# Optimization experiments

Measured on AMD Instinct MI355X. Metric: run time of the kernel, lower is better.

## Reference

```python
import jax, jax.numpy as jnp
import numpy as np

D = 1024
H = 16
HD = D // H
FF = 4 * D
EPS = 1e-5


def _layernorm(x, scale, shift):
    # Faithful to the torch module: unbiased std (ddof=1), eps added to std.
    mean = jnp.mean(x, axis=-1, keepdims=True)
    var = jnp.sum((x - mean) ** 2, axis=-1, keepdims=True) / (x.shape[-1] - 1)
    std = jnp.sqrt(var)
    return shift + scale * (x - mean) / (std + EPS)


def _gelu(x):
    c = jnp.sqrt(jnp.asarray(2.0 / jnp.pi, dtype=x.dtype))
    return 0.5 * x * (1.0 + jnp.tanh(c * (x + 0.044715 * x ** 3)))


def setup_inputs() -> dict:
    key = jax.random.key(0)
    ks = jax.random.split(key, 8)
    B, S = 2, 2048
    inv = 1.0 / np.sqrt(D)
    x = jax.random.normal(ks[0], (B, S, D), dtype=jnp.float32)
    scale1 = jnp.ones((D,), jnp.float32)
    shift1 = jnp.zeros((D,), jnp.float32)
    Wqkv = jax.random.normal(ks[1], (3 * D, D), jnp.float32) * inv  # torch layout [out,in]
    Wo_w = jax.random.normal(ks[2], (D, D), jnp.float32) * inv
    Wo_b = jnp.zeros((D,), jnp.float32)
    scale2 = jnp.ones((D,), jnp.float32)
    shift2 = jnp.zeros((D,), jnp.float32)
    W1 = jax.random.normal(ks[3], (FF, D), jnp.float32) * inv
    b1 = jnp.zeros((FF,), jnp.float32)
    W2 = jax.random.normal(ks[4], (D, FF), jnp.float32) * (1.0 / np.sqrt(FF))
    b2 = jnp.zeros((D,), jnp.float32)
    return {"x": x, "scale1": scale1, "shift1": shift1, "Wqkv": Wqkv,
            "Wo_w": Wo_w, "Wo_b": Wo_b, "scale2": scale2, "shift2": shift2,
            "W1": W1, "b1": b1, "W2": W2, "b2": b2}


def reference(x, scale1, shift1, Wqkv, Wo_w, Wo_b, scale2, shift2, W1, b1, W2, b2):
    B, S, _ = x.shape
    # --- pre-norm attention ---
    h = _layernorm(x, scale1, shift1)
    qkv = jnp.einsum('bsd,ed->bse', h, Wqkv)  # [B,S,3D]
    q, k, v = jnp.split(qkv, 3, axis=-1)
    q = q.reshape(B, S, H, HD).transpose(0, 2, 1, 3)  # [B,H,S,HD]
    k = k.reshape(B, S, H, HD).transpose(0, 2, 1, 3)
    v = v.reshape(B, S, H, HD).transpose(0, 2, 1, 3)
    scores = jnp.einsum('bhqd,bhkd->bhqk', q, k) / jnp.sqrt(jnp.asarray(HD, x.dtype))
    causal = jnp.triu(jnp.ones((S, S), dtype=bool), k=1)
    scores = jnp.where(causal, -jnp.inf, scores)
    weights = jax.nn.softmax(scores, axis=-1)
    attn = jnp.einsum('bhqk,bhkd->bhqd', weights, v)
    attn = attn.transpose(0, 2, 1, 3).reshape(B, S, D)
    attn = jnp.einsum('bsd,ed->bse', attn, Wo_w) + Wo_b
    x = x + attn
    # --- pre-norm MLP ---
    h2 = _layernorm(x, scale2, shift2)
    m = _gelu(jnp.einsum('bsd,fd->bsf', h2, W1) + b1)
    m = jnp.einsum('bsf,df->bsd', m, W2) + b2
    return x + m
```

## Files before the change

kernel.cpp:

```cpp
#include <hip/hip_runtime.h>
#include <cstdint>
#include <cstddef>

typedef __bf16 bf16;
typedef __bf16 v8bf __attribute__((ext_vector_type(8)));
typedef __bf16 v4bf __attribute__((ext_vector_type(4)));
typedef float  v4f  __attribute__((ext_vector_type(4)));

#define D_MODEL 1024
#define FF_DIM  4096
#define SEQ     2048
#define NTOK    4096
#define NH      16
#define HDIM    64

#define GLOAD_LDS16(g, l) \
    __builtin_amdgcn_global_load_lds((const __attribute__((address_space(1))) void*)(g), \
                                     (__attribute__((address_space(3))) void*)(l), 16, 0, 0)

#define QSCALE 0.18033688011112042f
#define SHIFT2 -28.853900817779268f

#define BARRIER()    asm volatile("s_barrier" ::: "memory")
#define WAIT_VM8()   asm volatile("s_waitcnt vmcnt(8)" ::: "memory")
#define WAIT_VM0()   asm volatile("s_waitcnt vmcnt(0)" ::: "memory")
#define WAIT_LGKM0() asm volatile("s_waitcnt lgkmcnt(0)" ::: "memory")

__global__ __launch_bounds__(256) void prep_kernel(
    const float* __restrict__ Wqkv, const float* __restrict__ Wo,
    const float* __restrict__ W1, const float* __restrict__ W2,
    bf16* __restrict__ Wqkv_b, bf16* __restrict__ Wo_b,
    bf16* __restrict__ W1_b, bf16* __restrict__ W2_b) {
    int u = blockIdx.x * 256 + threadIdx.x;
    const float* src; bf16* dst; int idx;
    if (u < 786432)       { src = Wqkv; dst = Wqkv_b; idx = u * 4; }
    else if (u < 1048576) { src = Wo;   dst = Wo_b;   idx = (u - 786432) * 4; }
    else if (u < 2097152) { src = W1;   dst = W1_b;   idx = (u - 1048576) * 4; }
    else                  { src = W2;   dst = W2_b;   idx = (u - 2097152) * 4; }
    float4 v = *(const float4*)(src + idx);
    dst[idx + 0] = (bf16)v.x;
    dst[idx + 1] = (bf16)v.y;
    dst[idx + 2] = (bf16)v.z;
    dst[idx + 3] = (bf16)v.w;
}

__global__ __launch_bounds__(256) void layernorm_kernel(
    const float* __restrict__ x, const float* __restrict__ scale,
    const float* __restrict__ shift, bf16* __restrict__ out) {
    int row = blockIdx.x;
    int t = threadIdx.x;
    const float* xr = x + (size_t)row * D_MODEL;
    float4 v = *(const float4*)(xr + t * 4);
    float s  = v.x + v.y + v.z + v.w;
    float sq = v.x * v.x + v.y * v.y + v.z * v.z + v.w * v.w;
    #pragma unroll
    for (int o = 1; o < 64; o <<= 1) {
        s  += __shfl_xor(s, o);
        sq += __shfl_xor(sq, o);
    }
    __shared__ float ws[8];
    int wv = t >> 6;
    if ((t & 63) == 0) { ws[wv * 2] = s; ws[wv * 2 + 1] = sq; }
    __syncthreads();
    s  = ws[0] + ws[2] + ws[4] + ws[6];
    sq = ws[1] + ws[3] + ws[5] + ws[7];
    float mean = s * (1.0f / D_MODEL);
    float var  = (sq - (float)D_MODEL * mean * mean) * (1.0f / (D_MODEL - 1));
    var = fmaxf(var, 0.0f);
    float inv = 1.0f / (sqrtf(var) + 1e-5f);
    #pragma unroll
    for (int j = 0; j < 4; ++j) {
        int c = t * 4 + j;
        float xv = (&v.x)[j];
        out[(size_t)row * D_MODEL + c] = (bf16)(shift[c] + scale[c] * (xv - mean) * inv);
    }
}

__global__ __launch_bounds__(256) void transpose_v(
    const bf16* __restrict__ vb, bf16* __restrict__ vt) {
    int bh = blockIdx.x >> 5;
    int ts = blockIdx.x & 31;
    int t = threadIdx.x;
    __shared__ bf16 T[64][72];
    const bf16* src = vb + ((size_t)bh * SEQ + ts * 64) * HDIM;
    #pragma unroll
    for (int half = 0; half < 2; ++half) {
        int s = (t >> 3) + half * 32;
        int d0 = (t & 7) * 8;
        v8bf vv = *(const v8bf*)(src + (size_t)s * HDIM + d0);
        #pragma unroll
        for (int j = 0; j < 8; ++j) T[d0 + j][s] = vv[j];
    }
    __syncthreads();
    bf16* dst = vt + (size_t)bh * HDIM * SEQ + ts * 64;
    int d = t >> 2;
    #pragma unroll
    for (int cc = 0; cc < 2; ++cc) {
        int c = (t & 3) + cc * 4;
        v8bf o = *(const v8bf*)(&T[d][c * 8]);
        *(v8bf*)(dst + (size_t)d * SEQ + c * 8) = o;
    }
}

template <int EPI>
__global__ __launch_bounds__(256) void gemm_nt(
    const bf16* __restrict__ A, const bf16* __restrict__ Bw,
    const float* __restrict__ bias, const float* __restrict__ resid,
    float* __restrict__ outf, bf16* __restrict__ ob0,
    bf16* __restrict__ ob1, bf16* __restrict__ ob2,
    int M, int N, int K, int klen) {
    __shared__ __align__(16) bf16 As[128 * 64];
    __shared__ __align__(16) bf16 Bs[128 * 64];
    int gx = gridDim.x;
    int lin = blockIdx.y * gx + blockIdx.x;
    int grpsz = 16 * gx;
    int group = lin / grpsz;
    int rem = lin - group * grpsz;
    int m_t = group * 16 + (rem & 15);
    int n_t = rem >> 4;
    int m0 = m_t * 128, n0 = n_t * 128;
    int kstart = blockIdx.z * klen;
    int t = threadIdx.x;
    int lane = t & 63, wave = t >> 6;
    int wm = wave >> 1, wn = wave & 1;
    int quad = lane >> 4, l16 = lane & 15;

    int srow8 = lane >> 3;
    int schunk = (lane & 7) ^ srow8;
    const bf16* agp = A  + (size_t)(m0 + wave * 8 + srow8) * K + kstart + schunk * 8;
    const bf16* bgp = Bw + (size_t)(n0 + wave * 8 + srow8) * K + kstart + schunk * 8;
    size_t row32 = (size_t)32 * K;

    v4f acc[4][4];
    #pragma unroll
    for (int i = 0; i < 4; ++i)
        #pragma unroll
        for (int j = 0; j < 4; ++j)
            acc[i][j] = (v4f){0.f, 0.f, 0.f, 0.f};

    int rsw = l16 & 7;
    for (int kk = 0; kk < klen; kk += 64) {
        __syncthreads();
        #pragma unroll
        for (int ii = 0; ii < 4; ++ii) {
            GLOAD_LDS16(agp + ii * row32 + kk, &As[ii * 2048 + wave * 512]);
            GLOAD_LDS16(bgp + ii * row32 + kk, &Bs[ii * 2048 + wave * 512]);
        }
        __syncthreads();
        #pragma unroll
        for (int h = 0; h < 2; ++h) {
            v8bf af[4], bfr[4];
            #pragma unroll
            for (int i = 0; i < 4; ++i)
                af[i] = *(const v8bf*)(&As[(wm * 64 + i * 16 + l16) * 64 + (((h * 4 + quad) ^ rsw)) * 8]);
            #pragma unroll
            for (int j = 0; j < 4; ++j)
                bfr[j] = *(const v8bf*)(&Bs[(wn * 64 + j * 16 + l16) * 64 + (((h * 4 + quad) ^ rsw)) * 8]);
            #pragma unroll
            for (int i = 0; i < 4; ++i)
                #pragma unroll
                for (int j = 0; j < 4; ++j)
                    acc[i][j] = __builtin_amdgcn_mfma_f32_16x16x32_bf16(af[i], bfr[j], acc[i][j], 0, 0, 0);
        }
    }

    #pragma unroll
    for (int i = 0; i < 4; ++i) {
        #pragma unroll
        for (int j = 0; j < 4; ++j) {
            #pragma unroll
            for (int r = 0; r < 4; ++r) {
                float v = acc[i][j][r];
                int row = m0 + wm * 64 + i * 16 + quad * 4 + r;
                int col = n0 + wn * 64 + j * 16 + l16;
                if (EPI == 1) {
                    size_t o = (size_t)row * N + col;
                    outf[o] = resid[o] + v + bias[col];
                }
            }
        }
    }
}

template <int EPI>
__global__ __launch_bounds__(512, 2) void gemm2_nt(
    const bf16* __restrict__ A, const bf16* __restrict__ Bw,
    const float* __restrict__ bias, bf16* __restrict__ ob0,
    bf16* __restrict__ ob1, bf16* __restrict__ ob2,
    int M, int N, int K, int klen) {
    __shared__ __align__(16) bf16 smA[2][256 * 64];
    __shared__ __align__(16) bf16 smB[2][256 * 64];

    int m0 = blockIdx.y * 256, n0 = blockIdx.x * 256;
    int kstart = blockIdx.z * klen;
    int t = threadIdx.x;
    int lane = t & 63, wave = t >> 6;
    int wm = wave >> 2, wn = wave & 3;
    int quad = lane >> 4, l16 = lane & 15;

    int srow8 = lane >> 3;
    int schunk = (lane & 7) ^ srow8;
    const bf16* aA = A  + (size_t)(m0 + wave * 8 + srow8) * K + kstart + schunk * 8;
    const bf16* bB = Bw + (size_t)(n0 + wave * 8 + srow8) * K + kstart + schunk * 8;
    size_t row64 = (size_t)64 * K;
    int NT = klen >> 6;

    v4f acc[8][4];
    #pragma unroll
    for (int i = 0; i < 8; ++i)
        #pragma unroll
        for (int j = 0; j < 4; ++j)
            acc[i][j] = (v4f){0.f, 0.f, 0.f, 0.f};

    auto stage = [&](int c, int kt) {
        size_t ko = (size_t)kt * 64;
        const bf16* ag = aA + ko;
        const bf16* bg = bB + ko;
        #pragma unroll
        for (int q = 0; q < 4; ++q) {
            GLOAD_LDS16(ag + q * row64, &smA[c][q * 4096 + wave * 512]);
            GLOAD_LDS16(bg + q * row64, &smB[c][q * 4096 + wave * 512]);
        }
    };

    stage(0, 0);
    if (NT > 1) { stage(1, 1); WAIT_VM8(); } else { WAIT_VM0(); }
    BARRIER();

    int rx = l16 & 7;
    int ch0 = (quad ^ rx) * 8;
    int ch1 = ch0 ^ 32;
    int arow = (wm * 128 + l16) * 64;
    int brow = (wn * 64 + l16) * 64;

    for (int kt = 0; kt < NT; ++kt) {
        int c = kt & 1;
        const bf16* Ab = &smA[c][arow];
        const bf16* Bb = &smB[c][brow];
        v8bf a[4][2], b[4][2];
        #pragma unroll
        for (int i = 0; i < 4; ++i) {
            a[i][0] = *(const v8bf*)(Ab + i * 1024 + ch0);
            a[i][1] = *(const v8bf*)(Ab + i * 1024 + ch1);
        }
        #pragma unroll
        for (int j = 0; j < 4; ++j) {
            b[j][0] = *(const v8bf*)(Bb + j * 1024 + ch0);
            b[j][1] = *(const v8bf*)(Bb + j * 1024 + ch1);
        }
        __builtin_amdgcn_s_setprio(1);
        #pragma unroll
        for (int i = 0; i < 4; ++i)
            #pragma unroll
            for (int j = 0; j < 2; ++j) {
                acc[i][j] = __builtin_amdgcn_mfma_f32_16x16x32_bf16(a[i][0], b[j][0], acc[i][j], 0, 0, 0);
                acc[i][j] = __builtin_amdgcn_mfma_f32_16x16x32_bf16(a[i][1], b[j][1], acc[i][j], 0, 0, 0);
            }
        __builtin_amdgcn_s_setprio(0);
        __builtin_amdgcn_s_setprio(1);
        #pragma unroll
        for (int i = 0; i < 4; ++i)
            #pragma unroll
            for (int j = 2; j < 4; ++j) {
                acc[i][j] = __builtin_amdgcn_mfma_f32_16x16x32_bf16(a[i][0], b[j][0], acc[i][j], 0, 0, 0);
                acc[i][j] = __builtin_amdgcn_mfma_f32_16x16x32_bf16(a[i][1], b[j][1], acc[i][j], 0, 0, 0);
            }
        __builtin_amdgcn_s_setprio(0);
        #pragma unroll
        for (int i = 0; i < 4; ++i) {
            a[i][0] = *(const v8bf*)(Ab + 4096 + i * 1024 + ch0);
            a[i][1] = *(const v8bf*)(Ab + 4096 + i * 1024 + ch1);
        }
        __builtin_amdgcn_s_setprio(1);
        #pragma unroll
        for (int i = 0; i < 4; ++i)
            #pragma unroll
            for (int j = 0; j < 2; ++j) {
                acc[i + 4][j] = __builtin_amdgcn_mfma_f32_16x16x32_bf16(a[i][0], b[j][0], acc[i + 4][j], 0, 0, 0);
                acc[i + 4][j] = __builtin_amdgcn_mfma_f32_16x16x32_bf16(a[i][1], b[j][1], acc[i + 4][j], 0, 0, 0);
            }
        __builtin_amdgcn_s_setprio(0);
        WAIT_LGKM0();
        BARRIER();
        if (kt + 2 < NT) stage(c, kt + 2);
        __builtin_amdgcn_s_setprio(1);
        #pragma unroll
        for (int i = 0; i < 4; ++i)
            #pragma unroll
            for (int j = 2; j < 4; ++j) {
                acc[i + 4][j] = __builtin_amdgcn_mfma_f32_16x16x32_bf16(a[i][0], b[j][0], acc[i + 4][j], 0, 0, 0);
                acc[i + 4][j] = __builtin_amdgcn_mfma_f32_16x16x32_bf16(a[i][1], b[j][1], acc[i + 4][j], 0, 0, 0);
            }
        __builtin_amdgcn_s_setprio(0);
        if (kt + 1 < NT) {
            if (kt + 2 < NT) WAIT_VM8();
            else             WAIT_VM0();
            BARRIER();
        }
    }

    #pragma unroll
    for (int i = 0; i < 8; ++i) {
        #pragma unroll
        for (int j = 0; j < 4; ++j) {
            #pragma unroll
            for (int r = 0; r < 4; ++r) {
                float v = acc[i][j][r];
                int row = m0 + wm * 128 + i * 16 + quad * 4 + r;
                int col = n0 + wn * 64 + j * 16 + l16;
                if (EPI == 0) {
                    int which = col >> 10, rr = col & 1023;
                    int h = rr >> 6, d = rr & 63;
                    int bb = row >> 11, sI = row & 2047;
                    size_t dst = (((size_t)(bb * NH + h)) * SEQ + sI) * HDIM + d;
                    if (which == 0)      ob0[dst] = (bf16)(v * QSCALE);
                    else if (which == 1) ob1[dst] = (bf16)v;
                    else                 ob2[dst] = (bf16)v;
                } else if (EPI == 2) {
                    float u = v + bias[col];
                    float y = 1.5957691216057308f * (u + 0.044715f * u * u * u);
                    float g = u * __builtin_amdgcn_rcpf(1.0f + __expf(-y));
                    ob0[(size_t)row * N + col] = (bf16)g;
                } else {
                    ob0[(size_t)blockIdx.z * M * N + (size_t)row * N + col] = (bf16)v;
                }
            }
        }
    }
}

__global__ __launch_bounds__(256) void combine_w2(
    const bf16* __restrict__ part, const float* __restrict__ x1,
    const float* __restrict__ b2, float* __restrict__ out) {
    int i = (blockIdx.x * 256 + threadIdx.x) * 4;
    int col = i & (D_MODEL - 1);
    float4 xv = *(const float4*)(x1 + i);
    float4 bv = *(const float4*)(b2 + col);
    float4 r;
    r.x = xv.x + bv.x; r.y = xv.y + bv.y; r.z = xv.z + bv.z; r.w = xv.w + bv.w;
    #pragma unroll
    for (int z = 0; z < 4; ++z) {
        v4bf p = *(const v4bf*)(part + (size_t)z * NTOK * D_MODEL + i);
        r.x += (float)p[0]; r.y += (float)p[1]; r.z += (float)p[2]; r.w += (float)p[3];
    }
    *(float4*)(out + i) = r;
}

__device__ __forceinline__ void attn_process_tile(
    int kv, int qwb, int quad, int l16,
    const bf16* Ks, const bf16* Vs, bf16* Pw, const v8bf& ones,
    const v8bf& qf0, const v8bf& qf1, v4f (&o)[4], v4f& o5) {
    #pragma unroll
    for (int hh = 0; hh < 2; ++hh) {
        int kb32 = kv + hh * 32;
        if (kb32 > qwb + 15) break;
        #pragma unroll
        for (int j2 = 0; j2 < 2; ++j2) {
            int j = hh * 2 + j2;
            int kb16 = kb32 + j2 * 16;
            union { bf16 h[4]; uint2 u; } pk;
            if (kb16 > qwb + 15) {
                pk.u = (uint2){0u, 0u};
            } else {
                int key = j * 16 + l16;
                v8bf ka = *(const v8bf*)(&Ks[(key * 8 + (quad ^ (key & 7))) * 8]);
                v8bf kc = *(const v8bf*)(&Ks[(key * 8 + ((quad + 4) ^ (key & 7))) * 8]);
                v4f s = (v4f){SHIFT2, SHIFT2, SHIFT2, SHIFT2};
                s = __builtin_amdgcn_mfma_f32_16x16x32_bf16(ka, qf0, s, 0, 0, 0);
                s = __builtin_amdgcn_mfma_f32_16x16x32_bf16(kc, qf1, s, 0, 0, 0);
                bool dm = (kb16 + 15 > qwb);
                int keyb = kb16 + quad * 4;
                #pragma unroll
                for (int r = 0; r < 4; ++r) {
                    float pv = __builtin_amdgcn_exp2f(s[r]);
                    if (dm) pv = (keyb + r <= qwb + l16) ? pv : 0.f;
                    pk.h[r] = (bf16)pv;
                }
            }
            *(uint2*)(&Pw[l16 * 80 + j * 16 + quad * 4]) = pk.u;
        }
        v8bf pf = *(const v8bf*)(&Pw[l16 * 80 + hh * 32 + quad * 8]);
        o5 = __builtin_amdgcn_mfma_f32_16x16x32_bf16(pf, ones, o5, 0, 0, 0);
        #pragma unroll
        for (int dc = 0; dc < 4; ++dc) {
            int dim = dc * 16 + l16;
            v8bf vv = *(const v8bf*)(&Vs[(dim * 8 + ((quad + 4 * hh) ^ (dim & 7))) * 8]);
            o[dc] = __builtin_amdgcn_mfma_f32_16x16x32_bf16(pf, vv, o[dc], 0, 0, 0);
        }
    }
}

__global__ __launch_bounds__(512, 4) void attn_kernel(
    const bf16* __restrict__ qb, const bf16* __restrict__ kb,
    const bf16* __restrict__ vt, bf16* __restrict__ ob) {
    int bh = blockIdx.x & 31;
    int pr = blockIdx.x >> 5;
    int qtA = pr, qtB = 31 - pr;

    int t = threadIdx.x;
    int wave = t >> 6, lane = t & 63;
    int g = wave >> 2, wv = wave & 3;
    int quad = lane >> 4, l16 = lane & 15;
    int qwbA = qtA * 64 + wv * 16;
    int qwbB = qtB * 64 + wv * 16;

    const bf16* Qh  = qb + (size_t)bh * SEQ * HDIM;
    const bf16* Kh  = kb + (size_t)bh * SEQ * HDIM;
    const bf16* Vth = vt + (size_t)bh * HDIM * SEQ;

    __shared__ __align__(16) char smem_raw[53248];
    bf16* Ks  = (bf16*)smem_raw;
    bf16* Vs  = (bf16*)(smem_raw + 16384);
    bf16* Pw  = (bf16*)(smem_raw + 32768) + wave * 1280;
    float* scr = (float*)smem_raw;

    int key = t >> 3;
    int cch = (t & 7) ^ (key & 7);
    const bf16* Ksrc = Kh + (size_t)key * HDIM + cch * 8;
    const bf16* Vsrc = Vth + (size_t)key * SEQ + cch * 8;
    bf16* kdst0 = Ks + wave * 512;
    bf16* kdst1 = Ks + 4096 + wave * 512;
    bf16* vdst0 = Vs + wave * 512;
    bf16* vdst1 = Vs + 4096 + wave * 512;

    v8bf qfA0 = *(const v8bf*)(Qh + (size_t)(qwbA + l16) * HDIM + quad * 8);
    v8bf qfA1 = *(const v8bf*)(Qh + (size_t)(qwbA + l16) * HDIM + 32 + quad * 8);
    v8bf qfB0 = *(const v8bf*)(Qh + (size_t)(qwbB + l16) * HDIM + quad * 8);
    v8bf qfB1 = *(const v8bf*)(Qh + (size_t)(qwbB + l16) * HDIM + 32 + quad * 8);

    v8bf ones;
    #pragma unroll
    for (int j = 0; j < 8; ++j) ones[j] = (bf16)1.0f;

    v4f oA[4], oB[4];
    #pragma unroll
    for (int dc = 0; dc < 4; ++dc) {
        oA[dc] = (v4f){0.f, 0.f, 0.f, 0.f};
        oB[dc] = (v4f){0.f, 0.f, 0.f, 0.f};
    }
    v4f o5A = (v4f){0.f, 0.f, 0.f, 0.f};
    v4f o5B = (v4f){0.f, 0.f, 0.f, 0.f};

    int nt = qtB + 1;
    int nit = (nt + 1) >> 1;
    for (int it = 0; it < nit; ++it) {
        int t0 = 2 * it;
        int t1 = t0 + 1;
        __syncthreads();
        GLOAD_LDS16(Ksrc + (size_t)(t0 * 64) * HDIM, kdst0);
        GLOAD_LDS16(Vsrc + t0 * 64, vdst0);
        if (t1 < nt) {
            GLOAD_LDS16(Ksrc + (size_t)(t1 * 64) * HDIM, kdst1);
            GLOAD_LDS16(Vsrc + t1 * 64, vdst1);
        }
        __syncthreads();
        int ti = t0 + g;
        if (ti < nt) {
            int kv = ti * 64;
            const bf16* Kst = Ks + g * 4096;
            const bf16* Vst = Vs + g * 4096;
            if (ti <= qtA)
                attn_process_tile(kv, qwbA, quad, l16, Kst, Vst, Pw, ones,
                                  qfA0, qfA1, oA, o5A);
            attn_process_tile(kv, qwbB, quad, l16, Kst, Vst, Pw, ones,
                              qfB0, qfB1, oB, o5B);
        }
    }

    __syncthreads();
    int sbase = wv * 2560 + lane;
    if (g == 1) {
        #pragma unroll
        for (int dc = 0; dc < 4; ++dc)
            #pragma unroll
            for (int r = 0; r < 4; ++r) {
                scr[sbase + (dc * 4 + r) * 64]        = oA[dc][r];
                scr[sbase + (16 + dc * 4 + r) * 64]   = oB[dc][r];
            }
        #pragma unroll
        for (int r = 0; r < 4; ++r) {
            scr[sbase + (32 + r) * 64] = o5A[r];
            scr[sbase + (36 + r) * 64] = o5B[r];
        }
    }
    __syncthreads();
    if (g == 0) {
        #pragma unroll
        for (int dc = 0; dc < 4; ++dc)
            #pragma unroll
            for (int r = 0; r < 4; ++r) {
                oA[dc][r] += scr[sbase + (dc * 4 + r) * 64];
                oB[dc][r] += scr[sbase + (16 + dc * 4 + r) * 64];
            }
        #pragma unroll
        for (int r = 0; r < 4; ++r) {
            o5A[r] += scr[sbase + (32 + r) * 64];
            o5B[r] += scr[sbase + (36 + r) * 64];
        }
        int b = bh >> 4, h = bh & 15;
        #pragma unroll
        for (int r = 0; r < 4; ++r) {
            float invA = 1.0f / o5A[r];
            float invB = 1.0f / o5B[r];
            int sA = qwbA + quad * 4 + r;
            int sB = qwbB + quad * 4 + r;
            #pragma unroll
            for (int dc = 0; dc < 4; ++dc) {
                int d = dc * 16 + l16;
                ob[((size_t)(b * SEQ + sA)) * D_MODEL + h * HDIM + d] = (bf16)(oA[dc][r] * invA);
                ob[((size_t)(b * SEQ + sB)) * D_MODEL + h * HDIM + d] = (bf16)(oB[dc][r] * invB);
            }
        }
    }
}

extern "C" void kernel_launch(void* const* d_in, const int* in_sizes, int n_in,
                              void* d_out, int out_size, void* d_ws, size_t ws_size,
                              hipStream_t stream) {
    const float* x      = (const float*)d_in[0];
    const float* scale1 = (const float*)d_in[1];
    const float* shift1 = (const float*)d_in[2];
    const float* Wqkv   = (const float*)d_in[3];
    const float* Wo_w   = (const float*)d_in[4];
    const float* Wo_b   = (const float*)d_in[5];
    const float* scale2 = (const float*)d_in[6];
    const float* shift2 = (const float*)d_in[7];
    const float* W1     = (const float*)d_in[8];
    const float* b1     = (const float*)d_in[9];
    const float* W2     = (const float*)d_in[10];
    const float* b2     = (const float*)d_in[11];
    float* out = (float*)d_out;

    char* ws = (char*)d_ws;
    size_t off = 0;
    auto alloc = [&](size_t bytes) -> char* {
        char* p = ws + off;
        off += (bytes + 255) & ~(size_t)255;
        return p;
    };
    bf16* Wqkv_b = (bf16*)alloc((size_t)3 * D_MODEL * D_MODEL * 2);
    bf16* Wo_bf  = (bf16*)alloc((size_t)D_MODEL * D_MODEL * 2);
    bf16* W1_b   = (bf16*)alloc((size_t)FF_DIM * D_MODEL * 2);
    bf16* W2_b   = (bf16*)alloc((size_t)D_MODEL * FF_DIM * 2);
    bf16* bufA   = (bf16*)alloc((size_t)NTOK * D_MODEL * 2);
    bf16* qb     = (bf16*)alloc((size_t)NTOK * D_MODEL * 2);
    bf16* kb     = (bf16*)alloc((size_t)NTOK * D_MODEL * 2);
    bf16* vb     = (bf16*)alloc((size_t)NTOK * D_MODEL * 2);
    bf16* vtb    = (bf16*)alloc((size_t)NTOK * D_MODEL * 2);
    float* x1    = (float*)alloc((size_t)NTOK * D_MODEL * 4);
    bf16* mbuf   = (bf16*)alloc((size_t)NTOK * FF_DIM * 2);
    bf16* w2part = bufA;
    (void)ws_size; (void)n_in; (void)in_sizes; (void)out_size;

    prep_kernel<<<12288, 256, 0, stream>>>(Wqkv, Wo_w, W1, W2,
                                           Wqkv_b, Wo_bf, W1_b, W2_b);

    layernorm_kernel<<<NTOK, 256, 0, stream>>>(x, scale1, shift1, bufA);

    gemm2_nt<0><<<dim3(3072 / 256, NTOK / 256), 512, 0, stream>>>(
        bufA, Wqkv_b, nullptr, qb, kb, vb, NTOK, 3072, D_MODEL, D_MODEL);

    transpose_v<<<1024, 256, 0, stream>>>(vb, vtb);

    attn_kernel<<<512, 512, 0, stream>>>(qb, kb, vtb, bufA);

    gemm_nt<1><<<dim3(D_MODEL / 128, NTOK / 128), 256, 0, stream>>>(
        bufA, Wo_bf, Wo_b, x, x1, nullptr, nullptr, nullptr, NTOK, D_MODEL, D_MODEL, D_MODEL);

    layernorm_kernel<<<NTOK, 256, 0, stream>>>(x1, scale2, shift2, qb);

    gemm2_nt<2><<<dim3(FF_DIM / 256, NTOK / 256), 512, 0, stream>>>(
        qb, W1_b, b1, mbuf, nullptr, nullptr, NTOK, FF_DIM, D_MODEL, D_MODEL);

    gemm2_nt<6><<<dim3(D_MODEL / 256, NTOK / 256, 4), 512, 0, stream>>>(
        mbuf, W2_b, nullptr, w2part, nullptr, nullptr, NTOK, D_MODEL, FF_DIM, FF_DIM / 4);

    combine_w2<<<NTOK * D_MODEL / 1024, 256, 0, stream>>>(w2part, x1, b2, out);
}
```

Before: 313.4 us.

## Software-pipeline attention K/V loads into registers and swizzle GEMM tile order

The attention kernel now preloads the first K/V tiles, then copies K and V fragments into registers so the next tiles' global-to-LDS loads can start right after a barrier. This overlaps memory traffic with the QK and PV MFMA work. Separate P buffers for the A and B query tiles grow LDS use to 68 KB, which may reduce occupancy. The gemm2_nt kernel also remaps block indices with an 8-way swizzle to improve L2 reuse.

```diff
diff --git a/kernel.cpp b/kernel.cpp
--- a/kernel.cpp
+++ b/kernel.cpp
@@ -191,7 +191,14 @@
     __shared__ __align__(16) bf16 smA[2][256 * 64];
     __shared__ __align__(16) bf16 smB[2][256 * 64];
 
-    int m0 = blockIdx.y * 256, n0 = blockIdx.x * 256;
+    int gx = gridDim.x, gy = gridDim.y;
+    int nwg = gx * gy;
+    int lin = blockIdx.y * gx + blockIdx.x;
+    int q8 = nwg >> 3;
+    int swz = (lin & 7) * q8 + (lin >> 3);
+    int m_t = swz % gy;
+    int n_t = swz / gy;
+    int m0 = m_t * 256, n0 = n_t * 256;
     int kstart = blockIdx.z * klen;
     int t = threadIdx.x;
     int lane = t & 63, wave = t >> 6;
@@ -346,50 +353,6 @@
     *(float4*)(out + i) = r;
 }
 
-__device__ __forceinline__ void attn_process_tile(
-    int kv, int qwb, int quad, int l16,
-    const bf16* Ks, const bf16* Vs, bf16* Pw, const v8bf& ones,
-    const v8bf& qf0, const v8bf& qf1, v4f (&o)[4], v4f& o5) {
-    #pragma unroll
-    for (int hh = 0; hh < 2; ++hh) {
-        int kb32 = kv + hh * 32;
-        if (kb32 > qwb + 15) break;
-        #pragma unroll
-        for (int j2 = 0; j2 < 2; ++j2) {
-            int j = hh * 2 + j2;
-            int kb16 = kb32 + j2 * 16;
-            union { bf16 h[4]; uint2 u; } pk;
-            if (kb16 > qwb + 15) {
-                pk.u = (uint2){0u, 0u};
-            } else {
-                int key = j * 16 + l16;
-                v8bf ka = *(const v8bf*)(&Ks[(key * 8 + (quad ^ (key & 7))) * 8]);
-                v8bf kc = *(const v8bf*)(&Ks[(key * 8 + ((quad + 4) ^ (key & 7))) * 8]);
-                v4f s = (v4f){SHIFT2, SHIFT2, SHIFT2, SHIFT2};
-                s = __builtin_amdgcn_mfma_f32_16x16x32_bf16(ka, qf0, s, 0, 0, 0);
-                s = __builtin_amdgcn_mfma_f32_16x16x32_bf16(kc, qf1, s, 0, 0, 0);
-                bool dm = (kb16 + 15 > qwb);
-                int keyb = kb16 + quad * 4;
-                #pragma unroll
-                for (int r = 0; r < 4; ++r) {
-                    float pv = __builtin_amdgcn_exp2f(s[r]);
-                    if (dm) pv = (keyb + r <= qwb + l16) ? pv : 0.f;
-                    pk.h[r] = (bf16)pv;
-                }
-            }
-            *(uint2*)(&Pw[l16 * 80 + j * 16 + quad * 4]) = pk.u;
-        }
-        v8bf pf = *(const v8bf*)(&Pw[l16 * 80 + hh * 32 + quad * 8]);
-        o5 = __builtin_amdgcn_mfma_f32_16x16x32_bf16(pf, ones, o5, 0, 0, 0);
-        #pragma unroll
-        for (int dc = 0; dc < 4; ++dc) {
-            int dim = dc * 16 + l16;
-            v8bf vv = *(const v8bf*)(&Vs[(dim * 8 + ((quad + 4 * hh) ^ (dim & 7))) * 8]);
-            o[dc] = __builtin_amdgcn_mfma_f32_16x16x32_bf16(pf, vv, o[dc], 0, 0, 0);
-        }
-    }
-}
-
 __global__ __launch_bounds__(512, 4) void attn_kernel(
     const bf16* __restrict__ qb, const bf16* __restrict__ kb,
     const bf16* __restrict__ vt, bf16* __restrict__ ob) {
@@ -408,10 +371,11 @@
     const bf16* Kh  = kb + (size_t)bh * SEQ * HDIM;
     const bf16* Vth = vt + (size_t)bh * HDIM * SEQ;
 
-    __shared__ __align__(16) char smem_raw[53248];
+    __shared__ __align__(16) char smem_raw[69632];
     bf16* Ks  = (bf16*)smem_raw;
     bf16* Vs  = (bf16*)(smem_raw + 16384);
-    bf16* Pw  = (bf16*)(smem_raw + 32768) + wave * 1280;
+    bf16* PwA = (bf16*)(smem_raw + 32768) + wave * 2304;
+    bf16* PwB = PwA + 1152;
     float* scr = (float*)smem_raw;
 
     int key = t >> 3;
@@ -441,30 +405,110 @@
     v4f o5A = (v4f){0.f, 0.f, 0.f, 0.f};
     v4f o5B = (v4f){0.f, 0.f, 0.f, 0.f};
 
+    const bf16* Kst = Ks + g * 4096;
+    const bf16* Vst = Vs + g * 4096;
+
     int nt = qtB + 1;
+    GLOAD_LDS16(Ksrc, kdst0);
+    GLOAD_LDS16(Ksrc + (size_t)64 * HDIM, kdst1);
+    GLOAD_LDS16(Vsrc, vdst0);
+    GLOAD_LDS16(Vsrc + 64, vdst1);
+    WAIT_VM0();
+    BARRIER();
+
     int nit = (nt + 1) >> 1;
     for (int it = 0; it < nit; ++it) {
-        int t0 = 2 * it;
-        int t1 = t0 + 1;
-        __syncthreads();
-        GLOAD_LDS16(Ksrc + (size_t)(t0 * 64) * HDIM, kdst0);
-        GLOAD_LDS16(Vsrc + t0 * 64, vdst0);
-        if (t1 < nt) {
-            GLOAD_LDS16(Ksrc + (size_t)(t1 * 64) * HDIM, kdst1);
-            GLOAD_LDS16(Vsrc + t1 * 64, vdst1);
-        }
-        __syncthreads();
-        int ti = t0 + g;
-        if (ti < nt) {
-            int kv = ti * 64;
-            const bf16* Kst = Ks + g * 4096;
-            const bf16* Vst = Vs + g * 4096;
-            if (ti <= qtA)
-                attn_process_tile(kv, qwbA, quad, l16, Kst, Vst, Pw, ones,
-                                  qfA0, qfA1, oA, o5A);
-            attn_process_tile(kv, qwbB, quad, l16, Kst, Vst, Pw, ones,
-                              qfB0, qfB1, oB, o5B);
-        }
+        int ti = 2 * it + g;
+        int kv = ti * 64;
+        bool act = (ti < nt);
+        bool doA = act && (ti <= qtA);
+        int nk0 = 2 * it + 2, nk1 = 2 * it + 3;
+
+        v8bf kr0[4], kr1[4];
+        if (act) {
+            #pragma unroll
+            for (int j = 0; j < 4; ++j) {
+                int ky = j * 16 + l16;
+                kr0[j] = *(const v8bf*)(&Kst[(ky * 8 + (quad ^ (ky & 7))) * 8]);
+                kr1[j] = *(const v8bf*)(&Kst[(ky * 8 + ((quad + 4) ^ (ky & 7))) * 8]);
+            }
+        }
+        WAIT_LGKM0();
+        BARRIER();
+        if (nk0 < nt) GLOAD_LDS16(Ksrc + (size_t)(nk0 * 64) * HDIM, kdst0);
+        if (nk1 < nt) GLOAD_LDS16(Ksrc + (size_t)(nk1 * 64) * HDIM, kdst1);
+
+        if (act) {
+            #pragma unroll
+            for (int sel = 0; sel < 2; ++sel) {
+                if (sel == 1 && !doA) break;
+                int qwb = sel ? qwbA : qwbB;
+                bf16* Pw = sel ? PwA : PwB;
+                const v8bf& q0 = sel ? qfA0 : qfB0;
+                const v8bf& q1 = sel ? qfA1 : qfB1;
+                bool skip1 = (kv + 32 > qwb + 15);
+                #pragma unroll
+                for (int j = 0; j < 4; ++j) {
+                    if (j >= 2 && skip1) continue;
+                    int kb16 = kv + j * 16;
+                    union { bf16 h[4]; uint2 u; } pk;
+                    if (kb16 > qwb + 15) {
+                        pk.u = (uint2){0u, 0u};
+                    } else {
+                        v4f s = (v4f){SHIFT2, SHIFT2, SHIFT2, SHIFT2};
+                        s = __builtin_amdgcn_mfma_f32_16x16x32_bf16(kr0[j], q0, s, 0, 0, 0);
+                        s = __builtin_amdgcn_mfma_f32_16x16x32_bf16(kr1[j], q1, s, 0, 0, 0);
+                        bool dm = (kb16 + 15 > qwb);
+                        int keyb = kb16 + quad * 4;
+                        #pragma unroll
+                        for (int r = 0; r < 4; ++r) {
+                            float pv = __builtin_amdgcn_exp2f(s[r]);
+                            if (dm) pv = (keyb + r <= qwb + l16) ? pv : 0.f;
+                            pk.h[r] = (bf16)pv;
+                        }
+                    }
+                    *(uint2*)(&Pw[l16 * 72 + j * 16 + quad * 4]) = pk.u;
+                }
+            }
+        }
+        __builtin_amdgcn_sched_barrier(0);
+
+        v8bf vr[2][4];
+        if (act) {
+            #pragma unroll
+            for (int hh = 0; hh < 2; ++hh)
+                #pragma unroll
+                for (int dc = 0; dc < 4; ++dc) {
+                    int dim = dc * 16 + l16;
+                    vr[hh][dc] = *(const v8bf*)(&Vst[(dim * 8 + ((quad + 4 * hh) ^ (dim & 7))) * 8]);
+                }
+        }
+        WAIT_LGKM0();
+        BARRIER();
+        if (nk0 < nt) GLOAD_LDS16(Vsrc + nk0 * 64, vdst0);
+        if (nk1 < nt) GLOAD_LDS16(Vsrc + nk1 * 64, vdst1);
+
+        if (act) {
+            #pragma unroll
+            for (int sel = 0; sel < 2; ++sel) {
+                if (sel == 1 && !doA) break;
+                int qwb = sel ? qwbA : qwbB;
+                bf16* Pw = sel ? PwA : PwB;
+                v4f* o = sel ? oA : oB;
+                v4f& o5 = sel ? o5A : o5B;
+                #pragma unroll
+                for (int hh = 0; hh < 2; ++hh) {
+                    if (kv + hh * 32 > qwb + 15) break;
+                    v8bf pf = *(const v8bf*)(&Pw[l16 * 72 + hh * 32 + quad * 8]);
+                    o5 = __builtin_amdgcn_mfma_f32_16x16x32_bf16(pf, ones, o5, 0, 0, 0);
+                    #pragma unroll
+                    for (int dc = 0; dc < 4; ++dc)
+                        o[dc] = __builtin_amdgcn_mfma_f32_16x16x32_bf16(pf, vr[hh][dc], o[dc], 0, 0, 0);
+                }
+            }
+        }
+        WAIT_VM0();
+        BARRIER();
     }
 
     __syncthreads();
```

Measured after the change: 442.2 us. 1.41x slower.
